# Kernel tuning notes

Measured on AMD Instinct MI355X. Metric: run time of the kernel, lower is better.

## Reference

```python
import jax, jax.numpy as jnp
import numpy as np

ALPHA = 1.0
BETTA = 1.0
WEIGHT_ROTE = 0.5
WEIGHT_MSE = 0.5
EPS_MASK = 1e-8

B, D = 16384, 768


def setup_inputs() -> dict:
    key = jax.random.key(0)
    k1, k2, k3, k4 = jax.random.split(key, 4)
    return {
        "init_img_vec": jax.random.normal(k1, (B, 1, D), dtype=jnp.float32),
        "next_img_vec": jax.random.normal(k2, (B, 1, D), dtype=jnp.float32),
        "init_unclip": jax.random.normal(k3, (B, 1, D), dtype=jnp.float32),
        "pred_unclip": jax.random.normal(k4, (B, 1, D), dtype=jnp.float32),
    }


def _transform_loss(init_img_vec, next_img_vec, init_unclip, pred_unclip):
    diff_img = (init_img_vec - next_img_vec)[:, 0, :].astype(jnp.float32)      # [B, D]
    diff_unclip = init_unclip[:, 0, :].astype(jnp.float32) - pred_unclip[:, 0, :]

    # mask-compaction: rows with ||diff_img|| > 1e-8 are kept. We keep the full
    # batch (jit-safe) and weight the batch-mean by the mask; identical result.
    norm1 = jnp.linalg.norm(diff_img, axis=-1, keepdims=True)                  # [B, 1]
    mask = (norm1 > EPS_MASK)                                                  # [B, 1]
    mask_f = mask.astype(jnp.float32)
    cnt = jnp.maximum(jnp.sum(mask_f), 1.0)

    v1 = jnp.where(mask, diff_img, 1.0)   # safe values on masked-out rows
    v2 = diff_unclip

    # RotationVectors.angle / unit_vector
    n1 = v1 / jnp.linalg.norm(v1, axis=-1, keepdims=True)                      # [B, D]
    norm2 = jnp.linalg.norm(v2, axis=-1, keepdims=True)
    cos_ang = jnp.clip(jnp.sum(v1 * v2, axis=-1, keepdims=True)
                       / (jnp.linalg.norm(v1, axis=-1, keepdims=True) * norm2),
                       -1.0, 1.0)
    a = jnp.arccos(cos_ang)                                                    # [B, 1]

    w = v2 - n1 * jnp.sum(n1 * v2, axis=-1, keepdims=True)
    n2 = w / jnp.linalg.norm(w, axis=-1, keepdims=True)                        # [B, D]

    sin_a = jnp.sin(a)                 # [B, 1]
    cos_a_m1 = jnp.cos(a) - 1.0        # [B, 1]

    # transform = alpha*sin_a*(n2 n1^T - n1 n2^T) + betta*(cos_a-1)*(n1 n1^T + n2 n2^T)
    # u_transform = transform @ ones ; (M v^T) @ 1 = M * sum(v), so no DxD needed.
    s1 = jnp.sum(n1, axis=-1, keepdims=True)   # n1 . u
    s2 = jnp.sum(n2, axis=-1, keepdims=True)   # n2 . u
    u_transform = (ALPHA * sin_a * (n2 * s1 - n1 * s2)
                   + BETTA * cos_a_m1 * (n1 * s1 + n2 * s2))                   # [B, D]

    # loss_u: MSE(u_transform, 0), mean over masked rows -> [D]
    loss_u = jnp.sum((u_transform ** 2) * mask_f, axis=0) / cnt
    # loss_I: MSE(I @ ones, ones) = 0 exactly -> [D]
    loss_I = jnp.zeros((diff_img.shape[-1],), dtype=jnp.float32)

    loss_u = jnp.nan_to_num(loss_u, nan=0.0, posinf=0.1, neginf=-0.1)
    loss_I = jnp.nan_to_num(loss_I, nan=0.0, posinf=0.1, neginf=-0.1)

    # plain MSE over the FULL (unmasked) batch, mean over dim 0 -> [D]
    mse = jnp.mean((diff_img - diff_unclip) ** 2, axis=0) + loss_I

    return WEIGHT_ROTE * loss_u, WEIGHT_MSE * mse


def reference(init_img_vec, next_img_vec, init_unclip, pred_unclip):
    return _transform_loss(init_img_vec, next_img_vec, init_unclip, pred_unclip)
```

## Files before the change

kernel.cpp:

```cpp
#include <hip/hip_runtime.h>
#include <math.h>


constexpr int D      = 768;
constexpr int B_ROWS = 16384;
constexpr int BDIM   = 256;
constexpr int NBLK   = 512;

__global__ void zero_ws_kernel(float* __restrict__ ws, int n) {
    int i = blockIdx.x * blockDim.x + threadIdx.x;
    if (i < n) ws[i] = 0.0f;
}

__global__ __launch_bounds__(BDIM) void transform_loss_main(
    const float* __restrict__ g_init_img,
    const float* __restrict__ g_next_img,
    const float* __restrict__ g_init_unclip,
    const float* __restrict__ g_pred_unclip,
    float* __restrict__ ws)
{
    const int lane  = threadIdx.x & 63;
    const int wave  = threadIdx.x >> 6;
    const int gwave = blockIdx.x * (BDIM / 64) + wave;
    const int nwav  = gridDim.x * (BDIM / 64);

    float acc_u[3][4];
    float acc_m[3][4];
#pragma unroll
    for (int t = 0; t < 3; ++t)
#pragma unroll
        for (int j = 0; j < 4; ++j) { acc_u[t][j] = 0.f; acc_m[t][j] = 0.f; }
    float local_cnt = 0.f;

    for (int row = gwave; row < B_ROWS; row += nwav) {
        const size_t base = (size_t)row * D + (size_t)(lane * 4);
        float4 va[3], vb[3], vc[3], vd[3];
#pragma unroll
        for (int t = 0; t < 3; ++t) {
            va[t] = *(const float4*)(g_init_img    + base + t * 256);
            vb[t] = *(const float4*)(g_next_img    + base + t * 256);
            vc[t] = *(const float4*)(g_init_unclip + base + t * 256);
            vd[t] = *(const float4*)(g_pred_unclip + base + t * 256);
        }
        float d1[3][4], d2[3][4];
        float sA = 0.f, sC = 0.f, sAB = 0.f, sS1 = 0.f, sS2 = 0.f;
#pragma unroll
        for (int t = 0; t < 3; ++t) {
            const float a4[4] = {va[t].x, va[t].y, va[t].z, va[t].w};
            const float b4[4] = {vb[t].x, vb[t].y, vb[t].z, vb[t].w};
            const float c4[4] = {vc[t].x, vc[t].y, vc[t].z, vc[t].w};
            const float e4[4] = {vd[t].x, vd[t].y, vd[t].z, vd[t].w};
#pragma unroll
            for (int j = 0; j < 4; ++j) {
                float x = a4[j] - b4[j];
                float y = c4[j] - e4[j];
                d1[t][j] = x; d2[t][j] = y;
                sA  = fmaf(x, x, sA);
                sC  = fmaf(y, y, sC);
                sAB = fmaf(x, y, sAB);
                sS1 += x;
                sS2 += y;
            }
        }
#pragma unroll
        for (int m = 1; m < 64; m <<= 1) {
            sA  += __shfl_xor(sA,  m);
            sC  += __shfl_xor(sC,  m);
            sAB += __shfl_xor(sAB, m);
            sS1 += __shfl_xor(sS1, m);
            sS2 += __shfl_xor(sS2, m);
        }

#pragma unroll
        for (int t = 0; t < 3; ++t)
#pragma unroll
            for (int j = 0; j < 4; ++j) {
                float dd = d1[t][j] - d2[t][j];
                acc_m[t][j] = fmaf(dd, dd, acc_m[t][j]);
            }

        const bool mask = (sA > 1e-16f);
        if (mask) {
            local_cnt += 1.f;
            float nA  = sqrtf(sA);
            float rA  = 1.f / nA;
            float nC  = sqrtf(sC);
            float cosang = sAB / (nA * nC);
            cosang = fminf(fmaxf(cosang, -1.f), 1.f);
            float sin_a = sqrtf(fmaxf(1.f - cosang * cosang, 0.f));
            float cm1 = cosang - 1.f;
            float k  = sAB / sA;
            float W  = sC - sAB * k;
            float rW = 1.f / sqrtf(W);
            float s1 = sS1 * rA;
            float s2 = (sS2 - sS1 * k) * rW;
            float p  = cm1 * s1 - sin_a * s2;
            float q  = sin_a * s1 + cm1 * s2;
            float c1 = p * rA - q * k * rW;
            float c2 = q * rW;
#pragma unroll
            for (int t = 0; t < 3; ++t)
#pragma unroll
                for (int j = 0; j < 4; ++j) {
                    float u = fmaf(d1[t][j], c1, d2[t][j] * c2);
                    acc_u[t][j] = fmaf(u, u, acc_u[t][j]);
                }
        }
    }

    __shared__ float sh[2 * D];
    __shared__ float shcnt;
    if (threadIdx.x == 0) shcnt = 0.f;
    for (int i = threadIdx.x; i < 2 * D; i += BDIM) sh[i] = 0.f;
    __syncthreads();
#pragma unroll
    for (int t = 0; t < 3; ++t)
#pragma unroll
        for (int j = 0; j < 4; ++j) {
            int dIdx = t * 256 + lane * 4 + j;
            atomicAdd(&sh[dIdx],     acc_u[t][j]);
            atomicAdd(&sh[D + dIdx], acc_m[t][j]);
        }
    if (lane == 0) atomicAdd(&shcnt, local_cnt);
    __syncthreads();
    for (int i = threadIdx.x; i < 2 * D; i += BDIM) atomicAdd(&ws[i], sh[i]);
    if (threadIdx.x == 0) atomicAdd(&ws[2 * D], shcnt);
}

__global__ void finalize_kernel(const float* __restrict__ ws, float* __restrict__ out) {
    int i = blockIdx.x * blockDim.x + threadIdx.x;
    if (i >= D) return;
    float cnt = fmaxf(ws[2 * D], 1.f);
    float lu = ws[i] / cnt;
    if (isnan(lu)) lu = 0.f;
    else if (isinf(lu)) lu = (lu > 0.f) ? 0.1f : -0.1f;
    out[i]     = 0.5f * lu;
    out[D + i] = 0.5f * (ws[D + i] * (1.f / 16384.f));
}

extern "C" void kernel_launch(void* const* d_in, const int* in_sizes, int n_in,
                              void* d_out, int out_size, void* d_ws, size_t ws_size,
                              hipStream_t stream) {
    const float* init_img    = (const float*)d_in[0];
    const float* next_img    = (const float*)d_in[1];
    const float* init_unclip = (const float*)d_in[2];
    const float* pred_unclip = (const float*)d_in[3];
    float* ws  = (float*)d_ws;
    float* out = (float*)d_out;

    zero_ws_kernel<<<(2 * D + 1 + BDIM - 1) / BDIM, BDIM, 0, stream>>>(ws, 2 * D + 1);
    transform_loss_main<<<NBLK, BDIM, 0, stream>>>(init_img, next_img, init_unclip,
                                                   pred_unclip, ws);
    finalize_kernel<<<(D + BDIM - 1) / BDIM, BDIM, 0, stream>>>(ws, out);
}
```

Measured before the change: 216.3 us.

## Prefetch next row, give each wave contiguous rows, replace global atomics with per-block partials

Each wave now handles a contiguous block of rows. It software-prefetches the next row's four float4 loads before the wave reduction of the current row, so memory latency overlaps with the shuffles. The grid doubles to 1024 blocks. When the workspace is large enough, each block writes its partial sums to a private slot instead of doing global atomics. A finalize kernel then reduces the 1024 partials, which also removes the zeroing kernel launch. The trade-offs are a larger workspace and a finalize pass that reads every partial with strided loads, plus higher register use from double-buffered inputs.

```diff
diff --git a/kernel.cpp b/kernel.cpp
--- a/kernel.cpp
+++ b/kernel.cpp
@@ -5,44 +5,48 @@
 constexpr int D      = 768;
 constexpr int B_ROWS = 16384;
 constexpr int BDIM   = 256;
-constexpr int NBLK   = 512;
+constexpr int NBLK   = 1024;
+constexpr int WPB    = BDIM / 64;
+constexpr int RPW    = B_ROWS / (NBLK * WPB);
+
 
 __global__ void zero_ws_kernel(float* __restrict__ ws, int n) {
     int i = blockIdx.x * blockDim.x + threadIdx.x;
     if (i < n) ws[i] = 0.0f;
 }
 
-__global__ __launch_bounds__(BDIM) void transform_loss_main(
-    const float* __restrict__ g_init_img,
-    const float* __restrict__ g_next_img,
-    const float* __restrict__ g_init_unclip,
-    const float* __restrict__ g_pred_unclip,
-    float* __restrict__ ws)
+template <bool PARTIALS>
+__global__ __launch_bounds__(BDIM)
+void transform_loss_main(const float* __restrict__ g_init_img,
+                         const float* __restrict__ g_next_img,
+                         const float* __restrict__ g_init_unclip,
+                         const float* __restrict__ g_pred_unclip,
+                         float* __restrict__ ws)
 {
     const int lane  = threadIdx.x & 63;
     const int wave  = threadIdx.x >> 6;
-    const int gwave = blockIdx.x * (BDIM / 64) + wave;
-    const int nwav  = gridDim.x * (BDIM / 64);
-
-    float acc_u[3][4];
-    float acc_m[3][4];
-#pragma unroll
-    for (int t = 0; t < 3; ++t)
-#pragma unroll
-        for (int j = 0; j < 4; ++j) { acc_u[t][j] = 0.f; acc_m[t][j] = 0.f; }
+    const int gwave = blockIdx.x * WPB + wave;
+    const int row0  = gwave * RPW;
+
+    float acc_u[12], acc_m[12];
+#pragma unroll
+    for (int i = 0; i < 12; ++i) { acc_u[i] = 0.f; acc_m[i] = 0.f; }
     float local_cnt = 0.f;
 
-    for (int row = gwave; row < B_ROWS; row += nwav) {
-        const size_t base = (size_t)row * D + (size_t)(lane * 4);
-        float4 va[3], vb[3], vc[3], vd[3];
-#pragma unroll
-        for (int t = 0; t < 3; ++t) {
-            va[t] = *(const float4*)(g_init_img    + base + t * 256);
-            vb[t] = *(const float4*)(g_next_img    + base + t * 256);
-            vc[t] = *(const float4*)(g_init_unclip + base + t * 256);
-            vd[t] = *(const float4*)(g_pred_unclip + base + t * 256);
-        }
-        float d1[3][4], d2[3][4];
+    const size_t base0 = (size_t)row0 * D + (size_t)(lane * 4);
+
+    float4 va[3], vb[3], vc[3], vd[3];
+#pragma unroll
+    for (int t = 0; t < 3; ++t) {
+        va[t] = *(const float4*)(g_init_img    + base0 + t * 256);
+        vb[t] = *(const float4*)(g_next_img    + base0 + t * 256);
+        vc[t] = *(const float4*)(g_init_unclip + base0 + t * 256);
+        vd[t] = *(const float4*)(g_pred_unclip + base0 + t * 256);
+    }
+
+#pragma unroll
+    for (int r = 0; r < RPW; ++r) {
+        float d1[12], d2[12];
         float sA = 0.f, sC = 0.f, sAB = 0.f, sS1 = 0.f, sS2 = 0.f;
 #pragma unroll
         for (int t = 0; t < 3; ++t) {
@@ -54,7 +58,7 @@
             for (int j = 0; j < 4; ++j) {
                 float x = a4[j] - b4[j];
                 float y = c4[j] - e4[j];
-                d1[t][j] = x; d2[t][j] = y;
+                d1[t * 4 + j] = x; d2[t * 4 + j] = y;
                 sA  = fmaf(x, x, sA);
                 sC  = fmaf(y, y, sC);
                 sAB = fmaf(x, y, sAB);
@@ -62,6 +66,16 @@
                 sS2 += y;
             }
         }
+        if (r + 1 < RPW) {
+            const size_t bn = base0 + (size_t)(r + 1) * D;
+#pragma unroll
+            for (int t = 0; t < 3; ++t) {
+                va[t] = *(const float4*)(g_init_img    + bn + t * 256);
+                vb[t] = *(const float4*)(g_next_img    + bn + t * 256);
+                vc[t] = *(const float4*)(g_init_unclip + bn + t * 256);
+                vd[t] = *(const float4*)(g_pred_unclip + bn + t * 256);
+            }
+        }
 #pragma unroll
         for (int m = 1; m < 64; m <<= 1) {
             sA  += __shfl_xor(sA,  m);
@@ -70,17 +84,12 @@
             sS1 += __shfl_xor(sS1, m);
             sS2 += __shfl_xor(sS2, m);
         }
-
-#pragma unroll
-        for (int t = 0; t < 3; ++t)
-#pragma unroll
-            for (int j = 0; j < 4; ++j) {
-                float dd = d1[t][j] - d2[t][j];
-                acc_m[t][j] = fmaf(dd, dd, acc_m[t][j]);
-            }
-
-        const bool mask = (sA > 1e-16f);
-        if (mask) {
+#pragma unroll
+        for (int i = 0; i < 12; ++i) {
+            float dd = d1[i] - d2[i];
+            acc_m[i] = fmaf(dd, dd, acc_m[i]);
+        }
+        if (sA > 1e-16f) {
             local_cnt += 1.f;
             float nA  = sqrtf(sA);
             float rA  = 1.f / nA;
@@ -99,12 +108,10 @@
             float c1 = p * rA - q * k * rW;
             float c2 = q * rW;
 #pragma unroll
-            for (int t = 0; t < 3; ++t)
-#pragma unroll
-                for (int j = 0; j < 4; ++j) {
-                    float u = fmaf(d1[t][j], c1, d2[t][j] * c2);
-                    acc_u[t][j] = fmaf(u, u, acc_u[t][j]);
-                }
+            for (int i = 0; i < 12; ++i) {
+                float u = fmaf(d1[i], c1, d2[i] * c2);
+                acc_u[i] = fmaf(u, u, acc_u[i]);
+            }
         }
     }
 
@@ -118,24 +125,63 @@
 #pragma unroll
         for (int j = 0; j < 4; ++j) {
             int dIdx = t * 256 + lane * 4 + j;
-            atomicAdd(&sh[dIdx],     acc_u[t][j]);
-            atomicAdd(&sh[D + dIdx], acc_m[t][j]);
+            atomicAdd(&sh[dIdx],     acc_u[t * 4 + j]);
+            atomicAdd(&sh[D + dIdx], acc_m[t * 4 + j]);
         }
     if (lane == 0) atomicAdd(&shcnt, local_cnt);
     __syncthreads();
-    for (int i = threadIdx.x; i < 2 * D; i += BDIM) atomicAdd(&ws[i], sh[i]);
-    if (threadIdx.x == 0) atomicAdd(&ws[2 * D], shcnt);
-}
-
-__global__ void finalize_kernel(const float* __restrict__ ws, float* __restrict__ out) {
-    int i = blockIdx.x * blockDim.x + threadIdx.x;
-    if (i >= D) return;
-    float cnt = fmaxf(ws[2 * D], 1.f);
-    float lu = ws[i] / cnt;
-    if (isnan(lu)) lu = 0.f;
-    else if (isinf(lu)) lu = (lu > 0.f) ? 0.1f : -0.1f;
-    out[i]     = 0.5f * lu;
-    out[D + i] = 0.5f * (ws[D + i] * (1.f / 16384.f));
+
+    if (PARTIALS) {
+        float* pb = ws + (size_t)blockIdx.x * (2 * D);
+        for (int i = threadIdx.x; i < 2 * D; i += BDIM) pb[i] = sh[i];
+        if (threadIdx.x == 0) ws[(size_t)NBLK * 2 * D + blockIdx.x] = shcnt;
+    } else {
+        for (int i = threadIdx.x; i < 2 * D; i += BDIM) atomicAdd(&ws[i], sh[i]);
+        if (threadIdx.x == 0) atomicAdd(&ws[2 * D], shcnt);
+    }
+}
+
+template <bool PARTIALS>
+__global__ __launch_bounds__(BDIM)
+void finalize_kernel(const float* __restrict__ ws, float* __restrict__ out)
+{
+    const int i = blockIdx.x * BDIM + threadIdx.x;
+    float cnt, s;
+    if (PARTIALS) {
+        float c = 0.f;
+        for (int r = threadIdx.x; r < NBLK; r += BDIM)
+            c += ws[(size_t)NBLK * 2 * D + r];
+#pragma unroll
+        for (int m = 1; m < 64; m <<= 1) c += __shfl_xor(c, m);
+        __shared__ float sc[WPB];
+        if ((threadIdx.x & 63) == 0) sc[threadIdx.x >> 6] = c;
+        __syncthreads();
+        c = 0.f;
+#pragma unroll
+        for (int wv = 0; wv < WPB; ++wv) c += sc[wv];
+        cnt = fmaxf(c, 1.f);
+
+        float s0 = 0.f, s1 = 0.f, s2 = 0.f, s3 = 0.f;
+        for (int r = 0; r < NBLK; r += 4) {
+            s0 += ws[(size_t)(r + 0) * 2 * D + i];
+            s1 += ws[(size_t)(r + 1) * 2 * D + i];
+            s2 += ws[(size_t)(r + 2) * 2 * D + i];
+            s3 += ws[(size_t)(r + 3) * 2 * D + i];
+        }
+        s = (s0 + s1) + (s2 + s3);
+    } else {
+        cnt = fmaxf(ws[2 * D], 1.f);
+        s = ws[i];
+    }
+
+    if (i < D) {
+        float lu = s / cnt;
+        if (isnan(lu)) lu = 0.f;
+        else if (isinf(lu)) lu = (lu > 0.f) ? 0.1f : -0.1f;
+        out[i] = 0.5f * lu;
+    } else {
+        out[i] = 0.5f * (s * (1.f / 16384.f));
+    }
 }
 
 extern "C" void kernel_launch(void* const* d_in, const int* in_sizes, int n_in,
@@ -148,8 +194,15 @@
     float* ws  = (float*)d_ws;
     float* out = (float*)d_out;
 
-    zero_ws_kernel<<<(2 * D + 1 + BDIM - 1) / BDIM, BDIM, 0, stream>>>(ws, 2 * D + 1);
-    transform_loss_main<<<NBLK, BDIM, 0, stream>>>(init_img, next_img, init_unclip,
-                                                   pred_unclip, ws);
-    finalize_kernel<<<(D + BDIM - 1) / BDIM, BDIM, 0, stream>>>(ws, out);
-}
+    const size_t need = ((size_t)NBLK * 2 * D + NBLK) * sizeof(float);
+    if (ws_size >= need) {
+        transform_loss_main<true><<<NBLK, BDIM, 0, stream>>>(
+            init_img, next_img, init_unclip, pred_unclip, ws);
+        finalize_kernel<true><<<(2 * D) / BDIM, BDIM, 0, stream>>>(ws, out);
+    } else {
+        zero_ws_kernel<<<(2 * D + 1 + BDIM - 1) / BDIM, BDIM, 0, stream>>>(ws, 2 * D + 1);
+        transform_loss_main<false><<<NBLK, BDIM, 0, stream>>>(
+            init_img, next_img, init_unclip, pred_unclip, ws);
+        finalize_kernel<false><<<(2 * D) / BDIM, BDIM, 0, stream>>>(ws, out);
+    }
+}
```

New measurement: 350.7 us. 62.1% more time.
